# Performance work log

Measured on AMD Instinct MI355X. Metric: run time of the kernel, lower is better.

The kernel has to match this reference:

```python
import jax, jax.numpy as jnp
import numpy as np

NUM_HEADS = 16
DIM_K = 64
EMB_DIM = 1024
NEG_INF = -1.0e9


def setup_inputs() -> dict:
    key = jax.random.key(0)
    ks = jax.random.split(key, 12)
    B, Sq, Skv, D = 2, 2048, 2048, EMB_DIM
    HDK = NUM_HEADS * DIM_K
    s = 1.0 / np.sqrt(D)
    return {
        "q": jax.random.normal(ks[0], (B, Sq, D), jnp.float32),
        "k": jax.random.normal(ks[1], (B, Skv, D), jnp.float32),
        "v": jax.random.normal(ks[2], (B, Skv, D), jnp.float32),
        "mask": jax.random.randint(ks[3], (B, 1, Skv), 0, 2, jnp.int32),
        "Wq": jax.random.normal(ks[4], (D, HDK), jnp.float32) * s,
        "bq": jnp.zeros((HDK,), jnp.float32),
        "Wk": jax.random.normal(ks[5], (D, HDK), jnp.float32) * s,
        "bk": jnp.zeros((HDK,), jnp.float32),
        "Wv": jax.random.normal(ks[6], (D, HDK), jnp.float32) * s,
        "bv": jnp.zeros((HDK,), jnp.float32),
        "Wo": jax.random.normal(ks[7], (HDK, D), jnp.float32) * (1.0 / np.sqrt(HDK)),
        "bo": jnp.zeros((D,), jnp.float32),
    }


def reference(q, k, v, mask, Wq, bq, Wk, bk, Wv, bv, Wo, bo):
    B, Sq, _ = q.shape
    Skv = k.shape[1]
    H, dk = NUM_HEADS, DIM_K
    # projections  (B,S,D) -> (B,H,S,dk)
    qh = (q @ Wq + bq).reshape(B, Sq, H, dk).transpose(0, 2, 1, 3)
    kh = (k @ Wk + bk).reshape(B, Skv, H, dk).transpose(0, 2, 1, 3)
    vh = (v @ Wv + bv).reshape(B, Skv, H, dk).transpose(0, 2, 1, 3)
    # scores (B,H,Sq,Skv)
    scores = jnp.einsum("bhqd,bhkd->bhqk", qh, kh) / jnp.float32(np.sqrt(dk))
    # mask (B,1,Skv) -> (B,1,1,Skv); masked_fill where mask == 0
    scores = jnp.where(mask[:, None] == 0, jnp.float32(NEG_INF), scores)
    probs = jax.nn.softmax(scores, axis=-1)  # dropout is identity in eval
    attn = jnp.einsum("bhqk,bhkd->bhqd", probs, vh)
    concat = attn.transpose(0, 2, 1, 3).reshape(B, Sq, H * dk)
    output = concat @ Wo + bo
    return output, scores
```

## Files before the change

### kernel.cpp

```cpp
#include <hip/hip_runtime.h>
#include <hip/hip_bf16.h>

typedef __attribute__((ext_vector_type(8))) short short8;
typedef __attribute__((ext_vector_type(4))) float f32x4;
typedef __hip_bfloat16 bf16;

typedef const void __attribute__((address_space(1))) as1_const_void;
typedef void __attribute__((address_space(3))) as3_void;

static __device__ __forceinline__ void gload_lds16(const bf16* g, bf16* l) {
    __builtin_amdgcn_global_load_lds((as1_const_void*)g, (as3_void*)l, 16, 0, 0);
}

#define NH 16
#define DK 64
#define SEQ 2048
#define DIM 1024
#define NEG_INF_F (-1.0e9f)

static __device__ __forceinline__ unsigned short f2bf_bits(float f) {
    bf16 t = __float2bfloat16(f);
    return *reinterpret_cast<unsigned short*>(&t);
}

__global__ void cvt_all_kernel(const float* __restrict__ q, const float* __restrict__ k,
                               const float* __restrict__ v, bf16* __restrict__ qb,
                               bf16* __restrict__ kb, bf16* __restrict__ vb) {
    const int N4 = 2 * SEQ * DIM / 4;
    int i = blockIdx.x * blockDim.x + threadIdx.x;
    int sel = i / N4, j = i - sel * N4;
    const float* in = (sel == 0) ? q : (sel == 1) ? k : v;
    bf16* out = (sel == 0) ? qb : (sel == 1) ? kb : vb;
    float4 x = reinterpret_cast<const float4*>(in)[j];
    ushort4 u;
    u.x = f2bf_bits(x.x);
    u.y = f2bf_bits(x.y);
    u.z = f2bf_bits(x.z);
    u.w = f2bf_bits(x.w);
    reinterpret_cast<ushort4*>(out)[j] = u;
}

__global__ void transpose_cvt_kernel(const float* __restrict__ Wq, const float* __restrict__ Wk,
                                     const float* __restrict__ Wv, const float* __restrict__ Wo,
                                     bf16* __restrict__ Wqt, bf16* __restrict__ Wkt,
                                     bf16* __restrict__ Wvt, bf16* __restrict__ Wot) {
    __shared__ float t[32][33];
    const int z = blockIdx.z;
    const float* W = (z == 0) ? Wq : (z == 1) ? Wk : (z == 2) ? Wv : Wo;
    bf16* Wt = (z == 0) ? Wqt : (z == 1) ? Wkt : (z == 2) ? Wvt : Wot;
    int n0 = blockIdx.x * 32, k0 = blockIdx.y * 32;
    int tx = threadIdx.x, ty = threadIdx.y;
#pragma unroll
    for (int i = 0; i < 4; i++)
        t[ty + i * 8][tx] = W[(size_t)(k0 + ty + i * 8) * DIM + n0 + tx];
    __syncthreads();
#pragma unroll
    for (int i = 0; i < 4; i++)
        Wt[(size_t)(n0 + ty + i * 8) * DIM + k0 + tx] = __float2bfloat16(t[tx][ty + i * 8]);
}

__global__ __launch_bounds__(256) void qkv_gemm_kernel(
    const bf16* __restrict__ qb, const bf16* __restrict__ kb, const bf16* __restrict__ vb,
    const bf16* __restrict__ Wcat,
    const float* __restrict__ bq, const float* __restrict__ bk, const float* __restrict__ bv,
    bf16* __restrict__ Qh, bf16* __restrict__ Kh, bf16* __restrict__ Vt)
{
    __shared__ __align__(16) bf16 Xs[2][128 * 32];
    __shared__ __align__(16) bf16 Ws[2][128 * 32];
    const int tid = threadIdx.x;
    const int w = tid >> 6, l = tid & 63;
    const int l15 = l & 15, l4 = l >> 4;
    const int lin = blockIdx.x;
    const int swz = (lin & 7) * 96 + (lin >> 3);
    const int proj = swz >> 8;
    const int rem = swz & 255;
    const int m0 = (rem >> 3) * 128;
    const int n0 = (rem & 7) * 128;
    const bf16* X = (proj == 0) ? qb : (proj == 1) ? kb : vb;
    const bf16* Wt = Wcat + (size_t)proj * DIM * DIM + (size_t)n0 * DIM;
    const float* bias = (proj == 0) ? bq : (proj == 1) ? bk : bv;
    const int wr = w >> 1, wc = w & 1;
    f32x4 acc[4][4] = {};

    const int c0 = tid, c1 = 256 + tid;
    const int r0 = c0 >> 2, ch0 = c0 & 3;
    const int r1 = c1 >> 2, ch1 = c1 & 3;
    const bf16* Xp = X + (size_t)m0 * DIM;

    gload_lds16(&Xp[(size_t)r0 * DIM + ch0 * 8], &Xs[0][c0 * 8]);
    gload_lds16(&Xp[(size_t)r1 * DIM + ch1 * 8], &Xs[0][c1 * 8]);
    gload_lds16(&Wt[(size_t)r0 * DIM + ch0 * 8], &Ws[0][c0 * 8]);
    gload_lds16(&Wt[(size_t)r1 * DIM + ch1 * 8], &Ws[0][c1 * 8]);
    __syncthreads();

    int cur = 0;
    for (int k0 = 0; k0 < DIM; k0 += 32) {
        if (k0 + 32 < DIM) {
            gload_lds16(&Xp[(size_t)r0 * DIM + k0 + 32 + ch0 * 8], &Xs[cur ^ 1][c0 * 8]);
            gload_lds16(&Xp[(size_t)r1 * DIM + k0 + 32 + ch1 * 8], &Xs[cur ^ 1][c1 * 8]);
            gload_lds16(&Wt[(size_t)r0 * DIM + k0 + 32 + ch0 * 8], &Ws[cur ^ 1][c0 * 8]);
            gload_lds16(&Wt[(size_t)r1 * DIM + k0 + 32 + ch1 * 8], &Ws[cur ^ 1][c1 * 8]);
        }
        short8 af[4], bfr[4];
#pragma unroll
        for (int mi = 0; mi < 4; mi++)
            af[mi] = *reinterpret_cast<const short8*>(&Xs[cur][(wr * 64 + mi * 16 + l15) * 32 + l4 * 8]);
#pragma unroll
        for (int ni = 0; ni < 4; ni++)
            bfr[ni] = *reinterpret_cast<const short8*>(&Ws[cur][(wc * 64 + ni * 16 + l15) * 32 + l4 * 8]);
#pragma unroll
        for (int mi = 0; mi < 4; mi++)
#pragma unroll
            for (int ni = 0; ni < 4; ni++)
                acc[mi][ni] = __builtin_amdgcn_mfma_f32_16x16x32_bf16(af[mi], bfr[ni], acc[mi][ni], 0, 0, 0);
        __syncthreads();
        cur ^= 1;
    }

#pragma unroll
    for (int mi = 0; mi < 4; mi++) {
#pragma unroll
        for (int ni = 0; ni < 4; ni++) {
            int n = n0 + wc * 64 + ni * 16 + l15;
            float bv = bias[n];
            int h = n >> 6, d = n & 63;
#pragma unroll
            for (int j = 0; j < 4; j++) {
                int m = m0 + wr * 64 + mi * 16 + l4 * 4 + j;
                float val = acc[mi][ni][j] + bv;
                int b = m >> 11, s = m & 2047;
                if (proj == 0)
                    Qh[((size_t)(b * NH + h) * SEQ + s) * DK + d] = __float2bfloat16(val * 0.125f);
                else if (proj == 1)
                    Kh[((size_t)(b * NH + h) * SEQ + s) * DK + d] = __float2bfloat16(val);
                else
                    Vt[((size_t)(b * NH + h) * DK + d) * SEQ + s] = __float2bfloat16(val);
            }
        }
    }
}

__global__ __launch_bounds__(256) void o_gemm_kernel(
    const bf16* __restrict__ X, const bf16* __restrict__ Wt,
    const float* __restrict__ bias, float* __restrict__ out)
{
    __shared__ __align__(16) bf16 Xs[2][64 * 32];
    __shared__ __align__(16) bf16 Ws[2][128 * 32];
    const int tid = threadIdx.x;
    const int w = tid >> 6, l = tid & 63;
    const int l15 = l & 15, l4 = l >> 4;
    const int lin = blockIdx.x;
    const int swz = (lin & 7) * 64 + (lin >> 3);
    const int m0 = (swz >> 3) * 64;
    const int n0 = (swz & 7) * 128;
    const int wr = w >> 1, wc = w & 1;
    f32x4 acc[2][4] = {};

    const int c0 = tid, c1 = 256 + tid;
    const int r0 = c0 >> 2, ch0 = c0 & 3;
    const int r1 = c1 >> 2, ch1 = c1 & 3;
    const bf16* Xp = X + (size_t)m0 * DIM;
    const bf16* Wp = Wt + (size_t)n0 * DIM;

    gload_lds16(&Xp[(size_t)r0 * DIM + ch0 * 8], &Xs[0][c0 * 8]);
    gload_lds16(&Wp[(size_t)r0 * DIM + ch0 * 8], &Ws[0][c0 * 8]);
    gload_lds16(&Wp[(size_t)r1 * DIM + ch1 * 8], &Ws[0][c1 * 8]);
    __syncthreads();

    int cur = 0;
    for (int k0 = 0; k0 < DIM; k0 += 32) {
        if (k0 + 32 < DIM) {
            gload_lds16(&Xp[(size_t)r0 * DIM + k0 + 32 + ch0 * 8], &Xs[cur ^ 1][c0 * 8]);
            gload_lds16(&Wp[(size_t)r0 * DIM + k0 + 32 + ch0 * 8], &Ws[cur ^ 1][c0 * 8]);
            gload_lds16(&Wp[(size_t)r1 * DIM + k0 + 32 + ch1 * 8], &Ws[cur ^ 1][c1 * 8]);
        }
        short8 af[2], bfr[4];
#pragma unroll
        for (int mi = 0; mi < 2; mi++)
            af[mi] = *reinterpret_cast<const short8*>(&Xs[cur][(wr * 32 + mi * 16 + l15) * 32 + l4 * 8]);
#pragma unroll
        for (int ni = 0; ni < 4; ni++)
            bfr[ni] = *reinterpret_cast<const short8*>(&Ws[cur][(wc * 64 + ni * 16 + l15) * 32 + l4 * 8]);
#pragma unroll
        for (int mi = 0; mi < 2; mi++)
#pragma unroll
            for (int ni = 0; ni < 4; ni++)
                acc[mi][ni] = __builtin_amdgcn_mfma_f32_16x16x32_bf16(af[mi], bfr[ni], acc[mi][ni], 0, 0, 0);
        __syncthreads();
        cur ^= 1;
    }

#pragma unroll
    for (int mi = 0; mi < 2; mi++) {
#pragma unroll
        for (int ni = 0; ni < 4; ni++) {
            int n = n0 + wc * 64 + ni * 16 + l15;
            float bv = bias[n];
#pragma unroll
            for (int j = 0; j < 4; j++) {
                int m = m0 + wr * 32 + mi * 16 + l4 * 4 + j;
                out[(size_t)m * DIM + n] = acc[mi][ni][j] + bv;
            }
        }
    }
}

__global__ __launch_bounds__(512) void attn_kernel(
    const bf16* __restrict__ Qh, const bf16* __restrict__ Kh,
    const bf16* __restrict__ Vt, const int* __restrict__ mask,
    float* __restrict__ scores, bf16* __restrict__ attn_c)
{
    __shared__ __align__(16) bf16 Ks[2][128 * 68];
    __shared__ __align__(16) bf16 Vs[2][64 * 132];
    __shared__ __align__(16) bf16 Ps[128 * 132];
    const int tid = threadIdx.x;
    const int w = tid >> 6, l = tid & 63;
    const int l15 = l & 15, l4 = l >> 4;
    const int lin = blockIdx.x;
    const int swz = (lin & 7) * 64 + (lin >> 3);
    const int bh = swz >> 4;
    const int q0 = (swz & 15) * 128;
    const int b = bh >> 4, h = bh & 15;
    const size_t head = (size_t)bh * SEQ * DK;

    const int ck0 = tid, ck1 = 512 + tid;
    const int kR0 = ck0 >> 3, kS0 = ck0 & 7;
    const int kR1 = ck1 >> 3, kS1 = ck1 & 7;
    const int vR0 = ck0 >> 4, vS0 = ck0 & 15;
    const int vR1 = ck1 >> 4, vS1 = ck1 & 15;

    const int* mrow = mask + b * SEQ;

    short8 aq[2];
#pragma unroll
    for (int ks = 0; ks < 2; ks++)
        aq[ks] = *reinterpret_cast<const short8*>(
            &Qh[head + (size_t)(q0 + w * 16 + l15) * DK + ks * 32 + l4 * 8]);

    {
        short8 k0v = *reinterpret_cast<const short8*>(&Kh[head + (size_t)kR0 * DK + kS0 * 8]);
        short8 k1v = *reinterpret_cast<const short8*>(&Kh[head + (size_t)kR1 * DK + kS1 * 8]);
        short8 v0v = *reinterpret_cast<const short8*>(&Vt[head + (size_t)vR0 * SEQ + vS0 * 8]);
        short8 v1v = *reinterpret_cast<const short8*>(&Vt[head + (size_t)vR1 * SEQ + vS1 * 8]);
        *reinterpret_cast<short8*>(&Ks[0][kR0 * 68 + kS0 * 8]) = k0v;
        *reinterpret_cast<short8*>(&Ks[0][kR1 * 68 + kS1 * 8]) = k1v;
        *reinterpret_cast<short8*>(&Vs[0][vR0 * 132 + vS0 * 8]) = v0v;
        *reinterpret_cast<short8*>(&Vs[0][vR1 * 132 + vS1 * 8]) = v1v;
    }
    __syncthreads();

    f32x4 oacc[4] = {};
    float mrun[4], lrun[4];
#pragma unroll
    for (int j = 0; j < 4; j++) { mrun[j] = -INFINITY; lrun[j] = 0.f; }

    int cur = 0;
    for (int t = 0; t < SEQ / 128; t++) {
        const int kv0 = t * 128;
        const bool more = t < (SEQ / 128 - 1);
        short8 nk0, nk1, nv0, nv1;
        if (more) {
            nk0 = *reinterpret_cast<const short8*>(&Kh[head + (size_t)(kv0 + 128 + kR0) * DK + kS0 * 8]);
            nk1 = *reinterpret_cast<const short8*>(&Kh[head + (size_t)(kv0 + 128 + kR1) * DK + kS1 * 8]);
            nv0 = *reinterpret_cast<const short8*>(&Vt[head + (size_t)vR0 * SEQ + kv0 + 128 + vS0 * 8]);
            nv1 = *reinterpret_cast<const short8*>(&Vt[head + (size_t)vR1 * SEQ + kv0 + 128 + vS1 * 8]);
        }

        f32x4 sacc[8] = {};
#pragma unroll
        for (int ks = 0; ks < 2; ks++) {
#pragma unroll
            for (int ni = 0; ni < 8; ni++) {
                short8 bk = *reinterpret_cast<const short8*>(
                    &Ks[cur][(ni * 16 + l15) * 68 + ks * 32 + l4 * 8]);
                sacc[ni] = __builtin_amdgcn_mfma_f32_16x16x32_bf16(aq[ks], bk, sacc[ni], 0, 0, 0);
            }
        }

#pragma unroll
        for (int ni = 0; ni < 8; ni++) {
            int mk = mrow[kv0 + ni * 16 + l15];
            if (mk == 0) {
#pragma unroll
                for (int j = 0; j < 4; j++) sacc[ni][j] = NEG_INF_F;
            }
        }

        {
            size_t base = ((size_t)bh * SEQ + q0 + w * 16) * SEQ + kv0;
#pragma unroll
            for (int j = 0; j < 4; j++) {
                size_t rb = base + (size_t)(l4 * 4 + j) * SEQ;
#pragma unroll
                for (int ni = 0; ni < 8; ni++)
                    __builtin_nontemporal_store(sacc[ni][j], &scores[rb + ni * 16 + l15]);
            }
        }

#pragma unroll
        for (int j = 0; j < 4; j++) {
            float mx = fmaxf(fmaxf(fmaxf(sacc[0][j], sacc[1][j]), fmaxf(sacc[2][j], sacc[3][j])),
                             fmaxf(fmaxf(sacc[4][j], sacc[5][j]), fmaxf(sacc[6][j], sacc[7][j])));
#pragma unroll
            for (int d = 1; d < 16; d <<= 1) mx = fmaxf(mx, __shfl_xor(mx, d));
            if (mx > mrun[j]) {
                float fac = __expf(mrun[j] - mx);
                lrun[j] *= fac;
#pragma unroll
                for (int ni = 0; ni < 4; ni++) oacc[ni][j] *= fac;
                mrun[j] = mx;
            }
            float mcur = mrun[j];
            float ps = 0.f;
#pragma unroll
            for (int ni = 0; ni < 8; ni++) {
                float p = __expf(sacc[ni][j] - mcur);
                sacc[ni][j] = p;
                ps += p;
            }
            lrun[j] += ps;
        }

#pragma unroll
        for (int j = 0; j < 4; j++) {
            int r = w * 16 + l4 * 4 + j;
#pragma unroll
            for (int ni = 0; ni < 8; ni++)
                Ps[r * 132 + ni * 16 + l15] = __float2bfloat16(sacc[ni][j]);
        }

#pragma unroll
        for (int ks = 0; ks < 4; ks++) {
            short8 pa = *reinterpret_cast<const short8*>(
                &Ps[(w * 16 + l15) * 132 + ks * 32 + l4 * 8]);
#pragma unroll
            for (int ni = 0; ni < 4; ni++) {
                short8 vbf = *reinterpret_cast<const short8*>(
                    &Vs[cur][(ni * 16 + l15) * 132 + ks * 32 + l4 * 8]);
                oacc[ni] = __builtin_amdgcn_mfma_f32_16x16x32_bf16(pa, vbf, oacc[ni], 0, 0, 0);
            }
        }

        if (more) {
            *reinterpret_cast<short8*>(&Ks[cur ^ 1][kR0 * 68 + kS0 * 8]) = nk0;
            *reinterpret_cast<short8*>(&Ks[cur ^ 1][kR1 * 68 + kS1 * 8]) = nk1;
            *reinterpret_cast<short8*>(&Vs[cur ^ 1][vR0 * 132 + vS0 * 8]) = nv0;
            *reinterpret_cast<short8*>(&Vs[cur ^ 1][vR1 * 132 + vS1 * 8]) = nv1;
        }
        __syncthreads();
        cur ^= 1;
    }

#pragma unroll
    for (int j = 0; j < 4; j++) {
        float ls = lrun[j];
#pragma unroll
        for (int d = 1; d < 16; d <<= 1) ls += __shfl_xor(ls, d);
        float inv = 1.f / ls;
        int s = q0 + w * 16 + l4 * 4 + j;
#pragma unroll
        for (int ni = 0; ni < 4; ni++)
            attn_c[((size_t)(b * SEQ + s)) * DIM + h * DK + ni * 16 + l15] =
                __float2bfloat16(oacc[ni][j] * inv);
    }
}

extern "C" void kernel_launch(void* const* d_in, const int* in_sizes, int n_in,
                              void* d_out, int out_size, void* d_ws, size_t ws_size,
                              hipStream_t stream)
{
    const float* q  = (const float*)d_in[0];
    const float* k  = (const float*)d_in[1];
    const float* v  = (const float*)d_in[2];
    const int*  msk = (const int*)d_in[3];
    const float* Wq = (const float*)d_in[4];
    const float* bq = (const float*)d_in[5];
    const float* Wk = (const float*)d_in[6];
    const float* bk = (const float*)d_in[7];
    const float* Wv = (const float*)d_in[8];
    const float* bv = (const float*)d_in[9];
    const float* Wo = (const float*)d_in[10];
    const float* bo = (const float*)d_in[11];

    const size_t MB = 1ull << 20;
    char* ws = (char*)d_ws;
    bf16* qb  = (bf16*)(ws + 0 * MB);
    bf16* kb  = (bf16*)(ws + 8 * MB);
    bf16* vb  = (bf16*)(ws + 16 * MB);
    bf16* Wqt = (bf16*)(ws + 24 * MB);
    bf16* Wkt = (bf16*)(ws + 26 * MB);
    bf16* Wvt = (bf16*)(ws + 28 * MB);
    bf16* Wot = (bf16*)(ws + 30 * MB);
    bf16* QhD = (bf16*)(ws + 32 * MB);
    bf16* KhD = (bf16*)(ws + 40 * MB);
    bf16* VtD = (bf16*)(ws + 48 * MB);
    bf16* att = (bf16*)(ws + 56 * MB);

    float* out = (float*)d_out;
    float* scores = out + (size_t)4096 * 1024;

    cvt_all_kernel<<<3 * 4096, 256, 0, stream>>>(q, k, v, qb, kb, vb);
    transpose_cvt_kernel<<<dim3(32, 32, 4), dim3(32, 8), 0, stream>>>(
        Wq, Wk, Wv, Wo, Wqt, Wkt, Wvt, Wot);

    qkv_gemm_kernel<<<768, 256, 0, stream>>>(qb, kb, vb, Wqt, bq, bk, bv, QhD, KhD, VtD);

    attn_kernel<<<512, 512, 0, stream>>>(QhD, KhD, VtD, msk, scores, att);

    o_gemm_kernel<<<512, 256, 0, stream>>>(att, Wot, bo, out);
}
```

Baseline: 221.3 us.

## Double attention query tile per block and merge prep kernels into one launch

Each attention block now processes 256 query rows (two 16-row MFMA sub-tiles per wave), reusing each staged K/V tile for twice as many MFMAs and halving the grid. The input conversion and weight transpose kernels are merged into a single launch dispatched on block index. This cuts K/V global and LDS traffic and one launch, at the cost of doubled register use for score accumulators and only one block per CU with fewer waves to hide latency.

```diff
diff --git a/kernel.cpp b/kernel.cpp
--- a/kernel.cpp
+++ b/kernel.cpp
@@ -23,40 +23,43 @@
     return *reinterpret_cast<unsigned short*>(&t);
 }
 
-__global__ void cvt_all_kernel(const float* __restrict__ q, const float* __restrict__ k,
-                               const float* __restrict__ v, bf16* __restrict__ qb,
-                               bf16* __restrict__ kb, bf16* __restrict__ vb) {
-    const int N4 = 2 * SEQ * DIM / 4;
-    int i = blockIdx.x * blockDim.x + threadIdx.x;
-    int sel = i / N4, j = i - sel * N4;
-    const float* in = (sel == 0) ? q : (sel == 1) ? k : v;
-    bf16* out = (sel == 0) ? qb : (sel == 1) ? kb : vb;
-    float4 x = reinterpret_cast<const float4*>(in)[j];
-    ushort4 u;
-    u.x = f2bf_bits(x.x);
-    u.y = f2bf_bits(x.y);
-    u.z = f2bf_bits(x.z);
-    u.w = f2bf_bits(x.w);
-    reinterpret_cast<ushort4*>(out)[j] = u;
-}
-
-__global__ void transpose_cvt_kernel(const float* __restrict__ Wq, const float* __restrict__ Wk,
-                                     const float* __restrict__ Wv, const float* __restrict__ Wo,
-                                     bf16* __restrict__ Wqt, bf16* __restrict__ Wkt,
-                                     bf16* __restrict__ Wvt, bf16* __restrict__ Wot) {
+__global__ void prep_kernel(const float* __restrict__ q, const float* __restrict__ k,
+                            const float* __restrict__ v, bf16* __restrict__ qb,
+                            bf16* __restrict__ kb, bf16* __restrict__ vb,
+                            const float* __restrict__ Wq, const float* __restrict__ Wk,
+                            const float* __restrict__ Wv, const float* __restrict__ Wo,
+                            bf16* __restrict__ Wqt, bf16* __restrict__ Wkt,
+                            bf16* __restrict__ Wvt, bf16* __restrict__ Wot) {
     __shared__ float t[32][33];
-    const int z = blockIdx.z;
-    const float* W = (z == 0) ? Wq : (z == 1) ? Wk : (z == 2) ? Wv : Wo;
-    bf16* Wt = (z == 0) ? Wqt : (z == 1) ? Wkt : (z == 2) ? Wvt : Wot;
-    int n0 = blockIdx.x * 32, k0 = blockIdx.y * 32;
-    int tx = threadIdx.x, ty = threadIdx.y;
-#pragma unroll
-    for (int i = 0; i < 4; i++)
-        t[ty + i * 8][tx] = W[(size_t)(k0 + ty + i * 8) * DIM + n0 + tx];
-    __syncthreads();
-#pragma unroll
-    for (int i = 0; i < 4; i++)
-        Wt[(size_t)(n0 + ty + i * 8) * DIM + k0 + tx] = __float2bfloat16(t[tx][ty + i * 8]);
+    const int tid = threadIdx.x;
+    if (blockIdx.x < 12288) {
+        const int N4 = 2 * SEQ * DIM / 4;
+        int i = blockIdx.x * 256 + tid;
+        int sel = i / N4, j = i - sel * N4;
+        const float* in = (sel == 0) ? q : (sel == 1) ? k : v;
+        bf16* out = (sel == 0) ? qb : (sel == 1) ? kb : vb;
+        float4 x = reinterpret_cast<const float4*>(in)[j];
+        ushort4 u;
+        u.x = f2bf_bits(x.x);
+        u.y = f2bf_bits(x.y);
+        u.z = f2bf_bits(x.z);
+        u.w = f2bf_bits(x.w);
+        reinterpret_cast<ushort4*>(out)[j] = u;
+    } else {
+        int bid = blockIdx.x - 12288;
+        int z = bid >> 10, rem = bid & 1023;
+        const float* W = (z == 0) ? Wq : (z == 1) ? Wk : (z == 2) ? Wv : Wo;
+        bf16* Wt = (z == 0) ? Wqt : (z == 1) ? Wkt : (z == 2) ? Wvt : Wot;
+        int n0 = (rem & 31) * 32, k0 = (rem >> 5) * 32;
+        int tx = tid & 31, ty = tid >> 5;
+#pragma unroll
+        for (int i = 0; i < 4; i++)
+            t[ty + i * 8][tx] = W[(size_t)(k0 + ty + i * 8) * DIM + n0 + tx];
+        __syncthreads();
+#pragma unroll
+        for (int i = 0; i < 4; i++)
+            Wt[(size_t)(n0 + ty + i * 8) * DIM + k0 + tx] = __float2bfloat16(t[tx][ty + i * 8]);
+    }
 }
 
 __global__ __launch_bounds__(256) void qkv_gemm_kernel(
@@ -212,14 +215,14 @@
 {
     __shared__ __align__(16) bf16 Ks[2][128 * 68];
     __shared__ __align__(16) bf16 Vs[2][64 * 132];
-    __shared__ __align__(16) bf16 Ps[128 * 132];
+    __shared__ __align__(16) bf16 Ps[256 * 132];
     const int tid = threadIdx.x;
     const int w = tid >> 6, l = tid & 63;
     const int l15 = l & 15, l4 = l >> 4;
     const int lin = blockIdx.x;
-    const int swz = (lin & 7) * 64 + (lin >> 3);
-    const int bh = swz >> 4;
-    const int q0 = (swz & 15) * 128;
+    const int swz = (lin & 7) * 32 + (lin >> 3);
+    const int bh = swz >> 3;
+    const int q0 = (swz & 7) * 256;
     const int b = bh >> 4, h = bh & 15;
     const size_t head = (size_t)bh * SEQ * DK;
 
@@ -231,11 +234,13 @@
 
     const int* mrow = mask + b * SEQ;
 
-    short8 aq[2];
-#pragma unroll
-    for (int ks = 0; ks < 2; ks++)
-        aq[ks] = *reinterpret_cast<const short8*>(
-            &Qh[head + (size_t)(q0 + w * 16 + l15) * DK + ks * 32 + l4 * 8]);
+    short8 aq[2][2];
+#pragma unroll
+    for (int mi = 0; mi < 2; mi++)
+#pragma unroll
+        for (int ks = 0; ks < 2; ks++)
+            aq[mi][ks] = *reinterpret_cast<const short8*>(
+                &Qh[head + (size_t)(q0 + w * 32 + mi * 16 + l15) * DK + ks * 32 + l4 * 8]);
 
     {
         short8 k0v = *reinterpret_cast<const short8*>(&Kh[head + (size_t)kR0 * DK + kS0 * 8]);
@@ -249,10 +254,12 @@
     }
     __syncthreads();
 
-    f32x4 oacc[4] = {};
-    float mrun[4], lrun[4];
-#pragma unroll
-    for (int j = 0; j < 4; j++) { mrun[j] = -INFINITY; lrun[j] = 0.f; }
+    f32x4 oacc[2][4] = {};
+    float mrun[2][4], lrun[2][4];
+#pragma unroll
+    for (int mi = 0; mi < 2; mi++)
+#pragma unroll
+        for (int j = 0; j < 4; j++) { mrun[mi][j] = -INFINITY; lrun[mi][j] = 0.f; }
 
     int cur = 0;
     for (int t = 0; t < SEQ / 128; t++) {
@@ -266,14 +273,16 @@
             nv1 = *reinterpret_cast<const short8*>(&Vt[head + (size_t)vR1 * SEQ + kv0 + 128 + vS1 * 8]);
         }
 
-        f32x4 sacc[8] = {};
+        f32x4 sacc[2][8] = {};
 #pragma unroll
         for (int ks = 0; ks < 2; ks++) {
 #pragma unroll
             for (int ni = 0; ni < 8; ni++) {
                 short8 bk = *reinterpret_cast<const short8*>(
                     &Ks[cur][(ni * 16 + l15) * 68 + ks * 32 + l4 * 8]);
-                sacc[ni] = __builtin_amdgcn_mfma_f32_16x16x32_bf16(aq[ks], bk, sacc[ni], 0, 0, 0);
+#pragma unroll
+                for (int mi = 0; mi < 2; mi++)
+                    sacc[mi][ni] = __builtin_amdgcn_mfma_f32_16x16x32_bf16(aq[mi][ks], bk, sacc[mi][ni], 0, 0, 0);
             }
         }
 
@@ -282,62 +291,74 @@
             int mk = mrow[kv0 + ni * 16 + l15];
             if (mk == 0) {
 #pragma unroll
-                for (int j = 0; j < 4; j++) sacc[ni][j] = NEG_INF_F;
-            }
-        }
-
-        {
-            size_t base = ((size_t)bh * SEQ + q0 + w * 16) * SEQ + kv0;
+                for (int mi = 0; mi < 2; mi++)
+#pragma unroll
+                    for (int j = 0; j < 4; j++) sacc[mi][ni][j] = NEG_INF_F;
+            }
+        }
+
+#pragma unroll
+        for (int mi = 0; mi < 2; mi++) {
+            size_t base = ((size_t)bh * SEQ + q0 + w * 32 + mi * 16) * SEQ + kv0;
 #pragma unroll
             for (int j = 0; j < 4; j++) {
                 size_t rb = base + (size_t)(l4 * 4 + j) * SEQ;
 #pragma unroll
                 for (int ni = 0; ni < 8; ni++)
-                    __builtin_nontemporal_store(sacc[ni][j], &scores[rb + ni * 16 + l15]);
-            }
-        }
-
-#pragma unroll
-        for (int j = 0; j < 4; j++) {
-            float mx = fmaxf(fmaxf(fmaxf(sacc[0][j], sacc[1][j]), fmaxf(sacc[2][j], sacc[3][j])),
-                             fmaxf(fmaxf(sacc[4][j], sacc[5][j]), fmaxf(sacc[6][j], sacc[7][j])));
-#pragma unroll
-            for (int d = 1; d < 16; d <<= 1) mx = fmaxf(mx, __shfl_xor(mx, d));
-            if (mx > mrun[j]) {
-                float fac = __expf(mrun[j] - mx);
-                lrun[j] *= fac;
-#pragma unroll
-                for (int ni = 0; ni < 4; ni++) oacc[ni][j] *= fac;
-                mrun[j] = mx;
-            }
-            float mcur = mrun[j];
-            float ps = 0.f;
-#pragma unroll
-            for (int ni = 0; ni < 8; ni++) {
-                float p = __expf(sacc[ni][j] - mcur);
-                sacc[ni][j] = p;
-                ps += p;
-            }
-            lrun[j] += ps;
-        }
-
-#pragma unroll
-        for (int j = 0; j < 4; j++) {
-            int r = w * 16 + l4 * 4 + j;
-#pragma unroll
-            for (int ni = 0; ni < 8; ni++)
-                Ps[r * 132 + ni * 16 + l15] = __float2bfloat16(sacc[ni][j]);
-        }
+                    __builtin_nontemporal_store(sacc[mi][ni][j], &scores[rb + ni * 16 + l15]);
+            }
+        }
+
+#pragma unroll
+        for (int mi = 0; mi < 2; mi++)
+#pragma unroll
+            for (int j = 0; j < 4; j++) {
+                float mx = fmaxf(fmaxf(fmaxf(sacc[mi][0][j], sacc[mi][1][j]), fmaxf(sacc[mi][2][j], sacc[mi][3][j])),
+                                 fmaxf(fmaxf(sacc[mi][4][j], sacc[mi][5][j]), fmaxf(sacc[mi][6][j], sacc[mi][7][j])));
+#pragma unroll
+                for (int d = 1; d < 16; d <<= 1) mx = fmaxf(mx, __shfl_xor(mx, d));
+                if (mx > mrun[mi][j]) {
+                    float fac = __expf(mrun[mi][j] - mx);
+                    lrun[mi][j] *= fac;
+#pragma unroll
+                    for (int ni = 0; ni < 4; ni++) oacc[mi][ni][j] *= fac;
+                    mrun[mi][j] = mx;
+                }
+                float mcur = mrun[mi][j];
+                float ps = 0.f;
+#pragma unroll
+                for (int ni = 0; ni < 8; ni++) {
+                    float p = __expf(sacc[mi][ni][j] - mcur);
+                    sacc[mi][ni][j] = p;
+                    ps += p;
+                }
+                lrun[mi][j] += ps;
+            }
+
+#pragma unroll
+        for (int mi = 0; mi < 2; mi++)
+#pragma unroll
+            for (int j = 0; j < 4; j++) {
+                int r = w * 32 + mi * 16 + l4 * 4 + j;
+#pragma unroll
+                for (int ni = 0; ni < 8; ni++)
+                    Ps[r * 132 + ni * 16 + l15] = __float2bfloat16(sacc[mi][ni][j]);
+            }
 
 #pragma unroll
         for (int ks = 0; ks < 4; ks++) {
-            short8 pa = *reinterpret_cast<const short8*>(
-                &Ps[(w * 16 + l15) * 132 + ks * 32 + l4 * 8]);
+            short8 pa[2];
+#pragma unroll
+            for (int mi = 0; mi < 2; mi++)
+                pa[mi] = *reinterpret_cast<const short8*>(
+                    &Ps[(w * 32 + mi * 16 + l15) * 132 + ks * 32 + l4 * 8]);
 #pragma unroll
             for (int ni = 0; ni < 4; ni++) {
                 short8 vbf = *reinterpret_cast<const short8*>(
                     &Vs[cur][(ni * 16 + l15) * 132 + ks * 32 + l4 * 8]);
-                oacc[ni] = __builtin_amdgcn_mfma_f32_16x16x32_bf16(pa, vbf, oacc[ni], 0, 0, 0);
+#pragma unroll
+                for (int mi = 0; mi < 2; mi++)
+                    oacc[mi][ni] = __builtin_amdgcn_mfma_f32_16x16x32_bf16(pa[mi], vbf, oacc[mi][ni], 0, 0, 0);
             }
         }
 
@@ -352,17 +373,19 @@
     }
 
 #pragma unroll
-    for (int j = 0; j < 4; j++) {
-        float ls = lrun[j];
-#pragma unroll
-        for (int d = 1; d < 16; d <<= 1) ls += __shfl_xor(ls, d);
-        float inv = 1.f / ls;
-        int s = q0 + w * 16 + l4 * 4 + j;
-#pragma unroll
-        for (int ni = 0; ni < 4; ni++)
-            attn_c[((size_t)(b * SEQ + s)) * DIM + h * DK + ni * 16 + l15] =
-                __float2bfloat16(oacc[ni][j] * inv);
-    }
+    for (int mi = 0; mi < 2; mi++)
+#pragma unroll
+        for (int j = 0; j < 4; j++) {
+            float ls = lrun[mi][j];
+#pragma unroll
+            for (int d = 1; d < 16; d <<= 1) ls += __shfl_xor(ls, d);
+            float inv = 1.f / ls;
+            int s = q0 + w * 32 + mi * 16 + l4 * 4 + j;
+#pragma unroll
+            for (int ni = 0; ni < 4; ni++)
+                attn_c[((size_t)(b * SEQ + s)) * DIM + h * DK + ni * 16 + l15] =
+                    __float2bfloat16(oacc[mi][ni][j] * inv);
+        }
 }
 
 extern "C" void kernel_launch(void* const* d_in, const int* in_sizes, int n_in,
@@ -399,13 +422,12 @@
     float* out = (float*)d_out;
     float* scores = out + (size_t)4096 * 1024;
 
-    cvt_all_kernel<<<3 * 4096, 256, 0, stream>>>(q, k, v, qb, kb, vb);
-    transpose_cvt_kernel<<<dim3(32, 32, 4), dim3(32, 8), 0, stream>>>(
-        Wq, Wk, Wv, Wo, Wqt, Wkt, Wvt, Wot);
+    prep_kernel<<<16384, 256, 0, stream>>>(q, k, v, qb, kb, vb,
+                                           Wq, Wk, Wv, Wo, Wqt, Wkt, Wvt, Wot);
 
     qkv_gemm_kernel<<<768, 256, 0, stream>>>(qb, kb, vb, Wqt, bq, bk, bv, QhD, KhD, VtD);
 
-    attn_kernel<<<512, 512, 0, stream>>>(QhD, KhD, VtD, msk, scores, att);
+    attn_kernel<<<256, 512, 0, stream>>>(QhD, KhD, VtD, msk, scores, att);
 
     o_gemm_kernel<<<512, 256, 0, stream>>>(att, Wot, bo, out);
 }
```

New measurement: 236.7 us. +7.0%, slower.
